# Kernel optimization log

Measured on AMD Instinct MI355X. Metric: run time of the kernel, lower is better.

Reference implementation:

```python
import jax, jax.numpy as jnp
import numpy as np

H, DK, DIM, DFF, DEPTH = 8, 64, 512, 2048, 8
B, LS, LT, VOCAB = 16, 128, 128, 32000


def setup_inputs() -> dict:
    key = jax.random.key(0)
    ks = jax.random.split(key, 20)
    w = lambda k, s: jax.random.normal(k, s, jnp.float32) * 0.02
    N_enc, N_dec = B * LS, B * LT
    base_s = np.arange(B) * LS
    base_t = np.arange(B) * LT
    i = np.arange(LS)
    j = np.arange(LT)
    # encoder self-attn: full bipartite within each sentence
    ee_src = (base_s[:, None, None] + i[None, :, None] + 0 * i[None, None, :]).reshape(-1)
    ee_dst = (base_s[:, None, None] + 0 * i[None, :, None] + i[None, None, :]).reshape(-1)
    # decoder self-attn: causal (key pos <= query pos)
    ii, jj = np.meshgrid(j, j, indexing='ij')  # ii = dst(query) pos, jj = src(key) pos
    m = jj <= ii
    dd_src = (base_t[:, None] + jj[m][None, :]).reshape(-1)
    dd_dst = (base_t[:, None] + ii[m][None, :]).reshape(-1)
    # cross-attn: enc node -> dec node, full within sentence
    ed_src = (base_s[:, None, None] + i[None, :, None] + 0 * j[None, None, :]).reshape(-1)
    ed_dst = (base_t[:, None, None] + 0 * i[None, :, None] + j[None, None, :]).reshape(-1)
    return {
        'emb_src': w(ks[0], (VOCAB, DIM)), 'emb_tgt': w(ks[1], (VOCAB, DIM)),
        'pos_emb': w(ks[2], (LS, DIM)), 'time_emb': w(ks[3], (DEPTH, DIM)),
        'Wqkv_e': w(ks[4], (DIM, 3 * DIM)), 'Wo_e': w(ks[5], (DIM, DIM)),
        'W1_e': w(ks[6], (DIM, DFF)), 'W2_e': w(ks[7], (DFF, DIM)),
        'Wqkv_d': w(ks[8], (DIM, 3 * DIM)), 'Wo_d': w(ks[9], (DIM, DIM)),
        'W1_d': w(ks[10], (DIM, DFF)), 'W2_d': w(ks[11], (DFF, DIM)),
        'Wq_x': w(ks[12], (DIM, DIM)), 'Wkv_x': w(ks[13], (DIM, 2 * DIM)),
        'Wo_x': w(ks[14], (DIM, DIM)), 'Wgen': w(ks[15], (DIM, VOCAB)),
        'src_tokens': jax.random.randint(ks[16], (N_enc,), 0, VOCAB, jnp.int32),
        'tgt_tokens': jax.random.randint(ks[17], (N_dec,), 0, VOCAB, jnp.int32),
        'src_pos': jnp.tile(jnp.arange(LS, dtype=jnp.int32), B),
        'tgt_pos': jnp.tile(jnp.arange(LT, dtype=jnp.int32), B),
        'ee_src': jnp.asarray(ee_src, jnp.int32), 'ee_dst': jnp.asarray(ee_dst, jnp.int32),
        'dd_src': jnp.asarray(dd_src, jnp.int32), 'dd_dst': jnp.asarray(dd_dst, jnp.int32),
        'ed_src': jnp.asarray(ed_src, jnp.int32), 'ed_dst': jnp.asarray(ed_dst, jnp.int32),
    }


def _ln(x):
    m = x.mean(-1, keepdims=True)
    v = ((x - m) ** 2).mean(-1, keepdims=True)
    return (x - m) * jax.lax.rsqrt(v + 1e-5)


def _attn(q, k, v, src, dst, n_dst):
    # q: [Nq,H,DK] (dst side), k/v: [Nk,H,DK] (src side); edge lists [E]
    # src_dot_dst -> scaled_exp -> scatter-sum (src_mul_edge + sum, copy_edge + sum), then wv/z
    s = jnp.exp(jnp.einsum('ehd,ehd->eh', k[src], q[dst]) / np.float32(np.sqrt(DK)))  # [E,H]
    wv = jax.ops.segment_sum(s[:, :, None] * v[src], dst, num_segments=n_dst)  # [Nq,H,DK]
    z = jax.ops.segment_sum(s, dst, num_segments=n_dst)  # [Nq,H]
    return (wv / (z[:, :, None] + 1e-9)).reshape(n_dst, DIM)


def reference(emb_src, emb_tgt, pos_emb, time_emb, Wqkv_e, Wo_e, W1_e, W2_e,
              Wqkv_d, Wo_d, W1_d, W2_d, Wq_x, Wkv_x, Wo_x, Wgen,
              src_tokens, tgt_tokens, src_pos, tgt_pos,
              ee_src, ee_dst, dd_src, dd_dst, ed_src, ed_dst):
    Ne, Nd = src_tokens.shape[0], tgt_tokens.shape[0]
    x_e = emb_src[src_tokens] + pos_emb[src_pos]
    x_d = emb_tgt[tgt_tokens] + pos_emb[tgt_pos]
    # encoder: MAX_DEPTH shared-weight iterations with time+pos enc re-added each step
    for t in range(DEPTH):
        xp = x_e + pos_emb[src_pos] + time_emb[t]
        q, k, v = jnp.split(xp @ Wqkv_e, 3, axis=-1)
        o = _attn(q.reshape(Ne, H, DK), k.reshape(Ne, H, DK), v.reshape(Ne, H, DK), ee_src, ee_dst, Ne)
        x_e = _ln(x_e + o @ Wo_e)
        x_e = _ln(x_e + jax.nn.relu(x_e @ W1_e) @ W2_e)
    # decoder: self-attn (causal dd) then cross-attn (ed) each iteration
    for t in range(DEPTH):
        xp = x_d + pos_emb[tgt_pos] + time_emb[t]
        q, k, v = jnp.split(xp @ Wqkv_d, 3, axis=-1)
        o = _attn(q.reshape(Nd, H, DK), k.reshape(Nd, H, DK), v.reshape(Nd, H, DK), dd_src, dd_dst, Nd)
        x_d = _ln(x_d + o @ Wo_d)
        qx = ((x_d + pos_emb[tgt_pos] + time_emb[t]) @ Wq_x).reshape(Nd, H, DK)
        kx, vx = jnp.split(x_e @ Wkv_x, 2, axis=-1)
        o = _attn(qx, kx.reshape(Ne, H, DK), vx.reshape(Ne, H, DK), ed_src, ed_dst, Nd)
        x_d = _ln(x_d + o @ Wo_x)
        x_d = _ln(x_d + jax.nn.relu(x_d @ W1_d) @ W2_d)
    return jax.nn.log_softmax(x_d @ Wgen, axis=-1)  # generator over dec nodes
```

## Files before the change

kernel.cpp:

```cpp
#include <hip/hip_runtime.h>
#include <hip/hip_bf16.h>
#include <math.h>

#define H 8
#define DK 64
#define DIM 512
#define DFF 2048
#define DEPTH 8
#define VOCAB 32000
#define NTOK 2048

typedef float f32x4 __attribute__((ext_vector_type(4)));
typedef short bf16x8 __attribute__((ext_vector_type(8)));

static __device__ __forceinline__ unsigned short f2bf(float f) {
    unsigned u = __float_as_uint(f);
    return (unsigned short)((u + 0x7FFFu + ((u >> 16) & 1u)) >> 16);
}

#define GLL(src, dst) __builtin_amdgcn_global_load_lds( \
    (const __attribute__((address_space(1))) unsigned int*)(src), \
    (__attribute__((address_space(3))) unsigned int*)(dst), 16, 0, 0)

__global__ void embed_kernel(const float* __restrict__ emb, const int* __restrict__ tok,
                             const float* __restrict__ pos, const int* __restrict__ pidx,
                             float* __restrict__ out, int n4) {
    int idx = blockIdx.x * blockDim.x + threadIdx.x;
    if (idx >= n4) return;
    int i = idx >> 7, d = idx & 127;
    float4 a = ((const float4*)emb)[(size_t)tok[i] * 128 + d];
    float4 b = ((const float4*)pos)[(size_t)pidx[i] * 128 + d];
    ((float4*)out)[idx] = make_float4(a.x + b.x, a.y + b.y, a.z + b.z, a.w + b.w);
}

struct WD { const float* src; unsigned short* dst; int K; int N; int t0; int pad; };
struct WTab { WD d[12]; };

__global__ __launch_bounds__(256) void wconv_all(WTab tab) {
    __shared__ float t[32][33];
    const int bid = blockIdx.x;
    int w = 0;
#pragma unroll
    for (int i = 1; i < 12; i++) if (bid >= tab.d[i].t0) w = i;
    const float* W = tab.d[w].src;
    unsigned short* Wt = tab.d[w].dst;
    const int K = tab.d[w].K, N = tab.d[w].N;
    const int lt = bid - tab.d[w].t0;
    const int txc = N >> 5;
    const int n0 = (lt % txc) << 5, k0 = (lt / txc) << 5;
    const int tid = threadIdx.x;
    const int tx = tid & 31, ty = tid >> 5;
#pragma unroll
    for (int i = 0; i < 32; i += 8)
        t[ty + i][tx] = W[(size_t)(k0 + ty + i) * N + n0 + tx];
    __syncthreads();
#pragma unroll
    for (int i = 0; i < 32; i += 8)
        Wt[(size_t)(n0 + ty + i) * K + k0 + tx] = f2bf(t[tx][ty + i]);
}

template<int EPI>
__global__ __launch_bounds__(256) void gemm_rb(
    const unsigned short* __restrict__ A,
    const unsigned short* __restrict__ Bt,
    unsigned short* __restrict__ Cb,
    int M, int N, int K)
{
    __shared__ __align__(16) unsigned short Asm[128 * 64];
    __shared__ __align__(16) unsigned short Bsm[128 * 64];
    const int tid = threadIdx.x;
    const int lane = tid & 63, wid = tid >> 6;
    const int m0 = blockIdx.y * 128, n0 = blockIdx.x * 128;
    const int wm = (wid >> 1) * 64, wn = (wid & 1) * 64;

    f32x4 acc[4][4];
#pragma unroll
    for (int i = 0; i < 4; i++)
#pragma unroll
        for (int j = 0; j < 4; j++) acc[i][j] = (f32x4){0.f, 0.f, 0.f, 0.f};

    for (int k0 = 0; k0 < K; k0 += 64) {
        if (k0) __syncthreads();
#pragma unroll
        for (int it = 0; it < 4; it++) {
            int q = (wid * 4 + it) * 64 + lane;
            int row = q >> 3;
            int cs = (q & 7) ^ (row & 7);
            GLL(Bt + (size_t)(n0 + row) * K + k0 + cs * 8, &Bsm[(wid * 4 + it) * 512]);
            GLL(A + (size_t)(m0 + row) * K + k0 + cs * 8, &Asm[(wid * 4 + it) * 512]);
        }
        __syncthreads();
#pragma unroll
        for (int kk = 0; kk < 2; kk++) {
            bf16x8 af[4], bfr[4];
#pragma unroll
            for (int i = 0; i < 4; i++) {
                int rowA = wm + i * 16 + (lane & 15);
                int ca = (kk * 4 + (lane >> 4)) ^ (rowA & 7);
                af[i] = *(const bf16x8*)&Asm[rowA * 64 + ca * 8];
                int rowB = wn + i * 16 + (lane & 15);
                int cb = (kk * 4 + (lane >> 4)) ^ (rowB & 7);
                bfr[i] = *(const bf16x8*)&Bsm[rowB * 64 + cb * 8];
            }
#pragma unroll
            for (int i = 0; i < 4; i++)
#pragma unroll
                for (int j = 0; j < 4; j++)
                    acc[i][j] = __builtin_amdgcn_mfma_f32_16x16x32_bf16(af[i], bfr[j], acc[i][j], 0, 0, 0);
        }
    }
#pragma unroll
    for (int i = 0; i < 4; i++)
#pragma unroll
        for (int j = 0; j < 4; j++)
#pragma unroll
            for (int r = 0; r < 4; r++) {
                int row = m0 + wm + i * 16 + (lane >> 4) * 4 + r;
                int col = n0 + wn + j * 16 + (lane & 15);
                size_t idx = (size_t)row * N + col;
                float v = acc[i][j][r];
                if (EPI == 1) Cb[idx] = f2bf(fmaxf(v, 0.f));
                if (EPI == 3) Cb[idx] = f2bf(v);
            }
}

__global__ __launch_bounds__(256) void gemm_bb(
    const unsigned short* __restrict__ A,
    const unsigned short* __restrict__ Bt,
    const float* __restrict__ R,
    float* __restrict__ Cf,
    int M, int N, int K)
{
    __shared__ __align__(16) unsigned short Asm[64 * 64];
    __shared__ __align__(16) unsigned short Bsm[64 * 64];
    const int tid = threadIdx.x;
    const int lane = tid & 63, wid = tid >> 6;
    const int m0 = blockIdx.y * 64, n0 = blockIdx.x * 64;
    const int wm = (wid >> 1) * 32, wn = (wid & 1) * 32;

    f32x4 acc[2][2];
#pragma unroll
    for (int i = 0; i < 2; i++)
#pragma unroll
        for (int j = 0; j < 2; j++) acc[i][j] = (f32x4){0.f, 0.f, 0.f, 0.f};

    for (int k0 = 0; k0 < K; k0 += 64) {
        if (k0) __syncthreads();
#pragma unroll
        for (int it = 0; it < 2; it++) {
            int q = it * 256 + tid;
            int row = q >> 3;
            int cs = (q & 7) ^ (row & 7);
            GLL(A + (size_t)(m0 + row) * K + k0 + cs * 8, &Asm[(it * 256 + wid * 64) * 8]);
            GLL(Bt + (size_t)(n0 + row) * K + k0 + cs * 8, &Bsm[(it * 256 + wid * 64) * 8]);
        }
        __syncthreads();
#pragma unroll
        for (int kd = 0; kd < 2; kd++) {
            bf16x8 af[2], bfr[2];
#pragma unroll
            for (int i = 0; i < 2; i++) {
                int rowA = wm + i * 16 + (lane & 15);
                int ca = (kd * 4 + (lane >> 4)) ^ (rowA & 7);
                af[i] = *(const bf16x8*)&Asm[rowA * 64 + ca * 8];
                int rowB = wn + i * 16 + (lane & 15);
                int cb = (kd * 4 + (lane >> 4)) ^ (rowB & 7);
                bfr[i] = *(const bf16x8*)&Bsm[rowB * 64 + cb * 8];
            }
#pragma unroll
            for (int i = 0; i < 2; i++)
#pragma unroll
                for (int j = 0; j < 2; j++)
                    acc[i][j] = __builtin_amdgcn_mfma_f32_16x16x32_bf16(af[i], bfr[j], acc[i][j], 0, 0, 0);
        }
    }
#pragma unroll
    for (int i = 0; i < 2; i++)
#pragma unroll
        for (int j = 0; j < 2; j++)
#pragma unroll
            for (int r = 0; r < 4; r++) {
                int row = m0 + wm + i * 16 + (lane >> 4) * 4 + r;
                int col = n0 + wn + j * 16 + (lane & 15);
                size_t idx = (size_t)row * N + col;
                Cf[idx] = acc[i][j][r] + R[idx];
            }
}

__global__ __launch_bounds__(64) void ln_kernel(const float* __restrict__ in,
                                                float* __restrict__ out,
                                                unsigned short* __restrict__ outb) {
    const int row = blockIdx.x, lane = threadIdx.x;
    const float* p = in + (size_t)row * DIM;
    float x[8];
#pragma unroll
    for (int i = 0; i < 8; i++) x[i] = p[lane + i * 64];
    float s = 0.f;
#pragma unroll
    for (int i = 0; i < 8; i++) s += x[i];
#pragma unroll
    for (int off = 32; off > 0; off >>= 1) s += __shfl_xor(s, off);
    const float m = s * (1.f / 512.f);
    float v = 0.f;
#pragma unroll
    for (int i = 0; i < 8; i++) { float d = x[i] - m; v += d * d; }
#pragma unroll
    for (int off = 32; off > 0; off >>= 1) v += __shfl_xor(v, off);
    v *= (1.f / 512.f);
    const float inv = 1.f / sqrtf(v + 1e-5f);
    float* q = out + (size_t)row * DIM;
    unsigned short* qb = outb + (size_t)row * DIM;
#pragma unroll
    for (int i = 0; i < 8; i++) {
        float y = (x[i] - m) * inv;
        q[lane + i * 64] = y;
        qb[lane + i * 64] = f2bf(y);
    }
}

template<int CAUSAL>
static __device__ __forceinline__ void attn_core16(
    const unsigned short* Qs, const unsigned short* Ks, const unsigned short* Vt,
    unsigned short* Psw, int wq, int lane, int tok0, int h,
    unsigned short* __restrict__ O)
{
    bf16x8 qa[2];
#pragma unroll
    for (int kd = 0; kd < 2; kd++) {
        int qr = wq + (lane & 15);
        int ch = (kd * 4 + (lane >> 4)) ^ (qr & 7);
        qa[kd] = *(const bf16x8*)&Qs[qr * 64 + ch * 8];
    }
    const int kcmax = CAUSAL ? ((wq >> 5) + 1) : 4;
    const int jmax = CAUSAL ? (kcmax * 2) : 8;

    float zr[4] = {0.f, 0.f, 0.f, 0.f};
    f32x4 oacc[4];
#pragma unroll
    for (int dt = 0; dt < 4; dt++) oacc[dt] = (f32x4){0.f, 0.f, 0.f, 0.f};

    for (int kb = 0; kb < 2; kb++) {
        int j0 = kb * 4;
        if (j0 >= jmax) break;
        int jn = jmax - j0; if (jn > 4) jn = 4;
        f32x4 sacc[4];
#pragma unroll
        for (int j = 0; j < 4; j++) sacc[j] = (f32x4){0.f, 0.f, 0.f, 0.f};
#pragma unroll 2
        for (int kd = 0; kd < 2; kd++) {
            for (int jj = 0; jj < jn; jj++) {
                int kr = (j0 + jj) * 16 + (lane & 15);
                int ch = (kd * 4 + (lane >> 4)) ^ (kr & 7);
                bf16x8 kf = *(const bf16x8*)&Ks[kr * 64 + ch * 8];
                sacc[jj] = __builtin_amdgcn_mfma_f32_16x16x32_bf16(qa[kd], kf, sacc[jj], 0, 0, 0);
            }
        }
        int qbase = wq + (lane >> 4) * 4;
        for (int jj = 0; jj < jn; jj++) {
            int kcol = (j0 + jj) * 16 + (lane & 15);
#pragma unroll
            for (int rr = 0; rr < 4; rr++) {
                float p = __expf(sacc[jj][rr] * 0.125f);
                if (CAUSAL && kcol > qbase + rr) p = 0.f;
                zr[rr] += p;
                int prow = (lane >> 4) * 4 + rr;
                int ch = ((jj * 2 + ((lane & 15) >> 3)) ^ (prow & 7));
                Psw[prow * 64 + ch * 8 + (lane & 7)] = f2bf(p);
            }
        }
        int kcn = kcmax - kb * 2; if (kcn > 2) kcn = 2;
        for (int kcl = 0; kcl < kcn; kcl++) {
            bf16x8 pa;
            {
                int prow = lane & 15;
                int ch = (kcl * 4 + (lane >> 4)) ^ (prow & 7);
                pa = *(const bf16x8*)&Psw[prow * 64 + ch * 8];
            }
            int kcg = kb * 2 + kcl;
#pragma unroll
            for (int dt = 0; dt < 4; dt++) {
                int d = dt * 16 + (lane & 15);
                bf16x8 vf = *(const bf16x8*)&Vt[d * 132 + (kcg * 4 + (lane >> 4)) * 8];
                oacc[dt] = __builtin_amdgcn_mfma_f32_16x16x32_bf16(pa, vf, oacc[dt], 0, 0, 0);
            }
        }
    }
#pragma unroll
    for (int rr = 0; rr < 4; rr++) {
        float z = zr[rr];
        z += __shfl_xor(z, 1); z += __shfl_xor(z, 2);
        z += __shfl_xor(z, 4); z += __shfl_xor(z, 8);
        zr[rr] = 1.f / (z + 1e-9f);
    }
#pragma unroll
    for (int dt = 0; dt < 4; dt++)
#pragma unroll
        for (int rr = 0; rr < 4; rr++) {
            int qrow = tok0 + wq + (lane >> 4) * 4 + rr;
            O[(size_t)qrow * DIM + h * 64 + dt * 16 + (lane & 15)] =
                f2bf(oacc[dt][rr] * zr[rr]);
        }
}

template<int CAUSAL>
__global__ __launch_bounds__(512) void fused_attn(
    const float* __restrict__ Xf,
    const float* __restrict__ pos,
    const float* __restrict__ trow,
    const unsigned short* __restrict__ WqkvT,
    unsigned short* __restrict__ O)
{
    __shared__ __align__(16) unsigned short smem[33024];
    unsigned short* Asm = smem;
    unsigned short* Bsm = smem + 8192;
    unsigned short* Qs  = smem;
    unsigned short* Ks  = smem + 8192;
    unsigned short* Vt  = smem + 16384;
    const int tid = threadIdx.x;
    const int lane = tid & 63, wid = tid >> 6;
    unsigned short* Psw = smem + 24832 + wid * 1024;
    const int b = blockIdx.x >> 3, h = blockIdx.x & 7;
    const int tok0 = b * 128;
    const int wq = wid * 16;

    f32x4 acc[12];
#pragma unroll
    for (int c = 0; c < 12; c++) acc[c] = (f32x4){0.f, 0.f, 0.f, 0.f};

    for (int k0 = 0; k0 < 512; k0 += 64) {
        if (k0) __syncthreads();
#pragma unroll
        for (int it = 0; it < 3; it++) {
            int q = it * 512 + wid * 64 + lane;
            int r = q >> 3;
            int cs = (q & 7) ^ (r & 7);
            int srow = (r < 64) ? (h * 64 + r)
                     : (r < 128) ? (512 + h * 64 + (r - 64))
                                 : (1024 + h * 64 + (r - 128));
            GLL(WqkvT + (size_t)srow * 512 + k0 + cs * 8, &Bsm[(it * 512 + wid * 64) * 8]);
        }
#pragma unroll
        for (int it = 0; it < 2; it++) {
            int q = it * 512 + tid;
            int row = q >> 3;
            int cs = q & 7;
            const float* s = Xf + (size_t)(tok0 + row) * 512 + k0 + cs * 8;
            const float* pp = pos + (size_t)row * 512 + k0 + cs * 8;
            const float* tt = trow + k0 + cs * 8;
            float4 u0 = *(const float4*)s, u1 = *(const float4*)(s + 4);
            float4 p0 = *(const float4*)pp, p1 = *(const float4*)(pp + 4);
            float4 t0 = *(const float4*)tt, t1 = *(const float4*)(tt + 4);
            u0.x += p0.x + t0.x; u0.y += p0.y + t0.y; u0.z += p0.z + t0.z; u0.w += p0.w + t0.w;
            u1.x += p1.x + t1.x; u1.y += p1.y + t1.y; u1.z += p1.z + t1.z; u1.w += p1.w + t1.w;
            unsigned short c8[8];
            c8[0] = f2bf(u0.x); c8[1] = f2bf(u0.y); c8[2] = f2bf(u0.z); c8[3] = f2bf(u0.w);
            c8[4] = f2bf(u1.x); c8[5] = f2bf(u1.y); c8[6] = f2bf(u1.z); c8[7] = f2bf(u1.w);
            *(bf16x8*)&Asm[row * 64 + ((cs ^ (row & 7)) * 8)] = *(bf16x8*)c8;
        }
        __syncthreads();
#pragma unroll
        for (int kk = 0; kk < 2; kk++) {
            int rowA = wq + (lane & 15);
            int ca = (kk * 4 + (lane >> 4)) ^ (rowA & 7);
            bf16x8 af = *(const bf16x8*)&Asm[rowA * 64 + ca * 8];
#pragma unroll
            for (int c = 0; c < 12; c++) {
                int rowB = c * 16 + (lane & 15);
                int cb = (kk * 4 + (lane >> 4)) ^ (rowB & 7);
                bf16x8 bfr = *(const bf16x8*)&Bsm[rowB * 64 + cb * 8];
                acc[c] = __builtin_amdgcn_mfma_f32_16x16x32_bf16(af, bfr, acc[c], 0, 0, 0);
            }
        }
    }
    __syncthreads();
#pragma unroll
    for (int c = 0; c < 12; c++)
#pragma unroll
        for (int r = 0; r < 4; r++) {
            int token = wq + (lane >> 4) * 4 + r;
            int col = (c & 3) * 16 + (lane & 15);
            unsigned short v = f2bf(acc[c][r]);
            if (c < 4)      Qs[token * 64 + (((col >> 3) ^ (token & 7)) * 8) + (col & 7)] = v;
            else if (c < 8) Ks[token * 64 + (((col >> 3) ^ (token & 7)) * 8) + (col & 7)] = v;
            else            Vt[col * 132 + token] = v;
        }
    __syncthreads();
    attn_core16<CAUSAL>(Qs, Ks, Vt, Psw, wq, lane, tok0, h, O);
}

__global__ __launch_bounds__(512) void fused_xattn(
    const float* __restrict__ Xf,
    const float* __restrict__ pos,
    const float* __restrict__ trow,
    const unsigned short* __restrict__ WqT,
    const unsigned short* __restrict__ kvx,
    unsigned short* __restrict__ O)
{
    __shared__ __align__(16) unsigned short smem[33024];
    unsigned short* Asm = smem;
    unsigned short* Bsm = smem + 8192;
    unsigned short* Qs  = smem;
    unsigned short* Ks  = smem + 8192;
    unsigned short* Vt  = smem + 16384;
    const int tid = threadIdx.x;
    const int lane = tid & 63, wid = tid >> 6;
    unsigned short* Psw = smem + 24832 + wid * 1024;
    const int b = blockIdx.x >> 3, h = blockIdx.x & 7;
    const int tok0 = b * 128;
    const int wq = wid * 16;

    f32x4 acc[4];
#pragma unroll
    for (int c = 0; c < 4; c++) acc[c] = (f32x4){0.f, 0.f, 0.f, 0.f};

    for (int k0 = 0; k0 < 512; k0 += 64) {
        if (k0) __syncthreads();
        {
            int q = wid * 64 + lane;
            int r = q >> 3;
            int cs = (q & 7) ^ (r & 7);
            GLL(WqT + (size_t)(h * 64 + r) * 512 + k0 + cs * 8, &Bsm[(wid * 64) * 8]);
        }
#pragma unroll
        for (int it = 0; it < 2; it++) {
            int q = it * 512 + tid;
            int row = q >> 3;
            int cs = q & 7;
            const float* s = Xf + (size_t)(tok0 + row) * 512 + k0 + cs * 8;
            const float* pp = pos + (size_t)row * 512 + k0 + cs * 8;
            const float* tt = trow + k0 + cs * 8;
            float4 u0 = *(const float4*)s, u1 = *(const float4*)(s + 4);
            float4 p0 = *(const float4*)pp, p1 = *(const float4*)(pp + 4);
            float4 t0 = *(const float4*)tt, t1 = *(const float4*)(tt + 4);
            u0.x += p0.x + t0.x; u0.y += p0.y + t0.y; u0.z += p0.z + t0.z; u0.w += p0.w + t0.w;
            u1.x += p1.x + t1.x; u1.y += p1.y + t1.y; u1.z += p1.z + t1.z; u1.w += p1.w + t1.w;
            unsigned short c8[8];
            c8[0] = f2bf(u0.x); c8[1] = f2bf(u0.y); c8[2] = f2bf(u0.z); c8[3] = f2bf(u0.w);
            c8[4] = f2bf(u1.x); c8[5] = f2bf(u1.y); c8[6] = f2bf(u1.z); c8[7] = f2bf(u1.w);
            *(bf16x8*)&Asm[row * 64 + ((cs ^ (row & 7)) * 8)] = *(bf16x8*)c8;
        }
        __syncthreads();
#pragma unroll
        for (int kk = 0; kk < 2; kk++) {
            int rowA = wq + (lane & 15);
            int ca = (kk * 4 + (lane >> 4)) ^ (rowA & 7);
            bf16x8 af = *(const bf16x8*)&Asm[rowA * 64 + ca * 8];
#pragma unroll
            for (int c = 0; c < 4; c++) {
                int rowB = c * 16 + (lane & 15);
                int cb = (kk * 4 + (lane >> 4)) ^ (rowB & 7);
                bf16x8 bfr = *(const bf16x8*)&Bsm[rowB * 64 + cb * 8];
                acc[c] = __builtin_amdgcn_mfma_f32_16x16x32_bf16(af, bfr, acc[c], 0, 0, 0);
            }
        }
    }
    __syncthreads();
#pragma unroll
    for (int c = 0; c < 4; c++)
#pragma unroll
        for (int r = 0; r < 4; r++) {
            int token = wq + (lane >> 4) * 4 + r;
            int col = c * 16 + (lane & 15);
            Qs[token * 64 + (((col >> 3) ^ (token & 7)) * 8) + (col & 7)] = f2bf(acc[c][r]);
        }
    {
        int r = tid >> 2, c0 = (tid & 3) * 2;
        const unsigned short* Kg = kvx + (size_t)(tok0 + r) * 1024 + h * 64;
        const unsigned short* Vg = Kg + 512;
#pragma unroll
        for (int c = c0; c < c0 + 2; c++) {
            bf16x8 kv = *(const bf16x8*)&Kg[c * 8];
            *(bf16x8*)&Ks[r * 64 + ((c ^ (r & 7)) * 8)] = kv;
            bf16x8 vv = *(const bf16x8*)&Vg[c * 8];
#pragma unroll
            for (int j = 0; j < 8; j++)
                Vt[(c * 8 + j) * 132 + r] = (unsigned short)vv[j];
        }
    }
    __syncthreads();
    attn_core16<0>(Qs, Ks, Vt, Psw, wq, lane, tok0, h, O);
}

__global__ __launch_bounds__(256) void gemm_gen(
    const unsigned short* __restrict__ Ab,
    const unsigned short* __restrict__ Bt,
    float* __restrict__ Out,
    float* __restrict__ pm,
    float* __restrict__ psum)
{
    __shared__ __align__(16) unsigned short Asm[128 * 64];
    __shared__ __align__(16) unsigned short Bsm[128 * 64];
    __shared__ float pml[4][64];
    __shared__ float psl[4][64];
    const int tid = threadIdx.x;
    const int lane = tid & 63, wid = tid >> 6;
    const int m0 = blockIdx.x * 128, n0 = blockIdx.y * 128;
    const int wm = (wid >> 1) * 64, wn = (wid & 1) * 64;

    f32x4 acc[4][4];
#pragma unroll
    for (int i = 0; i < 4; i++)
#pragma unroll
        for (int j = 0; j < 4; j++) acc[i][j] = (f32x4){0.f, 0.f, 0.f, 0.f};

    for (int k0 = 0; k0 < 512; k0 += 64) {
        if (k0) __syncthreads();
#pragma unroll
        for (int it = 0; it < 4; it++) {
            int q = (wid * 4 + it) * 64 + lane;
            int row = q >> 3;
            int cs = (q & 7) ^ (row & 7);
            GLL(Bt + (size_t)(n0 + row) * 512 + k0 + cs * 8, &Bsm[(wid * 4 + it) * 512]);
            GLL(Ab + (size_t)(m0 + row) * 512 + k0 + cs * 8, &Asm[(wid * 4 + it) * 512]);
        }
        __syncthreads();
#pragma unroll
        for (int kk = 0; kk < 2; kk++) {
            bf16x8 af[4], bfr[4];
#pragma unroll
            for (int i = 0; i < 4; i++) {
                int rowA = wm + i * 16 + (lane & 15);
                int ca = (kk * 4 + (lane >> 4)) ^ (rowA & 7);
                af[i] = *(const bf16x8*)&Asm[rowA * 64 + ca * 8];
                int rowB = wn + i * 16 + (lane & 15);
                int cb = (kk * 4 + (lane >> 4)) ^ (rowB & 7);
                bfr[i] = *(const bf16x8*)&Bsm[rowB * 64 + cb * 8];
            }
#pragma unroll
            for (int i = 0; i < 4; i++)
#pragma unroll
                for (int j = 0; j < 4; j++)
                    acc[i][j] = __builtin_amdgcn_mfma_f32_16x16x32_bf16(af[i], bfr[j], acc[i][j], 0, 0, 0);
        }
    }
#pragma unroll
    for (int i = 0; i < 4; i++) {
#pragma unroll
        for (int r = 0; r < 4; r++) {
            float mx = fmaxf(fmaxf(acc[i][0][r], acc[i][1][r]),
                             fmaxf(acc[i][2][r], acc[i][3][r]));
            mx = fmaxf(mx, __shfl_xor(mx, 1));
            mx = fmaxf(mx, __shfl_xor(mx, 2));
            mx = fmaxf(mx, __shfl_xor(mx, 4));
            mx = fmaxf(mx, __shfl_xor(mx, 8));
            float s = __expf(acc[i][0][r] - mx) + __expf(acc[i][1][r] - mx) +
                      __expf(acc[i][2][r] - mx) + __expf(acc[i][3][r] - mx);
            s += __shfl_xor(s, 1); s += __shfl_xor(s, 2);
            s += __shfl_xor(s, 4); s += __shfl_xor(s, 8);
            if ((lane & 15) == 0) {
                int li = i * 16 + (lane >> 4) * 4 + r;
                pml[wid][li] = mx;
                psl[wid][li] = s;
            }
        }
    }
    __syncthreads();
    if (tid < 128) {
        int half = tid >> 6, lr = tid & 63;
        int wa = half * 2, wb = half * 2 + 1;
        float ma = pml[wa][lr], mb = pml[wb][lr];
        float m = fmaxf(ma, mb);
        float s = psl[wa][lr] * __expf(ma - m) + psl[wb][lr] * __expf(mb - m);
        pm[(size_t)(m0 + tid) * 256 + blockIdx.y] = m;
        psum[(size_t)(m0 + tid) * 256 + blockIdx.y] = s;
    }
#pragma unroll
    for (int i = 0; i < 4; i++)
#pragma unroll
        for (int j = 0; j < 4; j++)
#pragma unroll
            for (int r = 0; r < 4; r++) {
                int row = m0 + wm + i * 16 + (lane >> 4) * 4 + r;
                int col = n0 + wn + j * 16 + (lane & 15);
                Out[(size_t)row * VOCAB + col] = acc[i][j][r];
            }
}

__global__ __launch_bounds__(64) void lse_kernel(const float* __restrict__ pm,
                                                 const float* __restrict__ psum,
                                                 float* __restrict__ lse) {
    const int row = blockIdx.x, t = threadIdx.x;
    float m = -1e30f, s = 0.f;
    for (int nb = t; nb < 250; nb += 64) {
        float mm = pm[(size_t)row * 256 + nb];
        float ss = psum[(size_t)row * 256 + nb];
        float M = fmaxf(m, mm);
        s = s * __expf(m - M) + ss * __expf(mm - M);
        m = M;
    }
#pragma unroll
    for (int off = 32; off > 0; off >>= 1) {
        float mo = __shfl_xor(m, off), so = __shfl_xor(s, off);
        float M = fmaxf(m, mo);
        s = s * __expf(m - M) + so * __expf(mo - M);
        m = M;
    }
    if (t == 0) lse[row] = m + __logf(s);
}

__global__ __launch_bounds__(256) void sub_kernel(float* __restrict__ out,
                                                  const float* __restrict__ lse) {
    const int row = blockIdx.x;
    const float l = lse[row];
    float4* p = (float4*)(out + (size_t)row * VOCAB);
    for (int i = threadIdx.x; i < VOCAB / 4; i += 256) {
        float4 v = p[i];
        p[i] = make_float4(v.x - l, v.y - l, v.z - l, v.w - l);
    }
}

extern "C" void kernel_launch(void* const* d_in, const int* in_sizes, int n_in,
                              void* d_out, int out_size, void* d_ws, size_t ws_size,
                              hipStream_t stream) {
    const float* emb_src  = (const float*)d_in[0];
    const float* emb_tgt  = (const float*)d_in[1];
    const float* pos_emb  = (const float*)d_in[2];
    const float* time_emb = (const float*)d_in[3];
    const float* Wqkv_e   = (const float*)d_in[4];
    const float* Wo_e     = (const float*)d_in[5];
    const float* W1_e     = (const float*)d_in[6];
    const float* W2_e     = (const float*)d_in[7];
    const float* Wqkv_d   = (const float*)d_in[8];
    const float* Wo_d     = (const float*)d_in[9];
    const float* W1_d     = (const float*)d_in[10];
    const float* W2_d     = (const float*)d_in[11];
    const float* Wq_x     = (const float*)d_in[12];
    const float* Wkv_x    = (const float*)d_in[13];
    const float* Wo_x     = (const float*)d_in[14];
    const float* Wgen     = (const float*)d_in[15];
    const int* src_tokens = (const int*)d_in[16];
    const int* tgt_tokens = (const int*)d_in[17];
    const int* src_pos    = (const int*)d_in[18];
    const int* tgt_pos    = (const int*)d_in[19];

    char* w = (char*)d_ws;
    float* x_e = (float*)(w);
    float* x_d = (float*)(w + (4u << 20));
    float* tmp = (float*)(w + (8u << 20));
    unsigned short* kvx_bf = (unsigned short*)(w + (12u << 20));
    unsigned short* o_bf   = (unsigned short*)(w + (16u << 20));
    unsigned short* hid_bf = (unsigned short*)(w + (18u << 20));
    float* pm   = (float*)(w + (26u << 20));
    float* psum = (float*)(w + (28u << 20));
    float* lse  = (float*)(w + (30u << 20));
    unsigned short* xe_bf = (unsigned short*)(w + (31u << 20));
    unsigned short* xd_bf = (unsigned short*)(w + (33u << 20));
    unsigned short* wts   = (unsigned short*)(w + (35u << 20));

    unsigned short* WqkvE_t = wts;
    unsigned short* WoE_t   = WqkvE_t + 786432;
    unsigned short* W1E_t   = WoE_t   + 262144;
    unsigned short* W2E_t   = W1E_t   + 1048576;
    unsigned short* WqkvD_t = W2E_t   + 1048576;
    unsigned short* WoD_t   = WqkvD_t + 786432;
    unsigned short* W1D_t   = WoD_t   + 262144;
    unsigned short* W2D_t   = W1D_t   + 1048576;
    unsigned short* WqX_t   = W2D_t   + 1048576;
    unsigned short* WkvX_t  = WqX_t   + 262144;
    unsigned short* WoX_t   = WkvX_t  + 524288;
    unsigned short* Wgen_t  = WoX_t   + 262144;

    float* out = (float*)d_out;

    WTab tab;
    auto set = [&](int i, const float* s, unsigned short* d, int K, int N, int t0) {
        tab.d[i].src = s; tab.d[i].dst = d; tab.d[i].K = K; tab.d[i].N = N;
        tab.d[i].t0 = t0; tab.d[i].pad = 0;
    };
    set(0,  Wqkv_e, WqkvE_t, 512, 1536, 0);
    set(1,  Wo_e,   WoE_t,   512, 512,  768);
    set(2,  W1_e,   W1E_t,   512, 2048, 1024);
    set(3,  W2_e,   W2E_t,   2048, 512, 2048);
    set(4,  Wqkv_d, WqkvD_t, 512, 1536, 3072);
    set(5,  Wo_d,   WoD_t,   512, 512,  3840);
    set(6,  W1_d,   W1D_t,   512, 2048, 4096);
    set(7,  W2_d,   W2D_t,   2048, 512, 5120);
    set(8,  Wq_x,   WqX_t,   512, 512,  6144);
    set(9,  Wkv_x,  WkvX_t,  512, 1024, 6400);
    set(10, Wo_x,   WoX_t,   512, 512,  6912);
    set(11, Wgen,   Wgen_t,  512, 32000, 7168);
    wconv_all<<<23168, 256, 0, stream>>>(tab);

    const int n4 = NTOK * (DIM / 4);
    dim3 eb(256), eg((n4 + 255) / 256);
    embed_kernel<<<eg, eb, 0, stream>>>(emb_src, src_tokens, pos_emb, src_pos, x_e, n4);
    embed_kernel<<<eg, eb, 0, stream>>>(emb_tgt, tgt_tokens, pos_emb, tgt_pos, x_d, n4);

    const dim3 gFF(DFF / 128, NTOK / 128), gKV(1024 / 128, NTOK / 128),
               g64(512 / 64, NTOK / 64);

    for (int t = 0; t < DEPTH; t++) {
        const float* trow = time_emb + (size_t)t * DIM;
        fused_attn<0><<<128, 512, 0, stream>>>(x_e, pos_emb, trow, WqkvE_t, o_bf);
        gemm_bb<<<g64, 256, 0, stream>>>(o_bf, WoE_t, x_e, tmp, NTOK, 512, 512);
        ln_kernel<<<NTOK, 64, 0, stream>>>(tmp, x_e, xe_bf);
        gemm_rb<1><<<gFF, 256, 0, stream>>>(xe_bf, W1E_t, hid_bf, NTOK, DFF, 512);
        gemm_bb<<<g64, 256, 0, stream>>>(hid_bf, W2E_t, x_e, tmp, NTOK, 512, 2048);
        ln_kernel<<<NTOK, 64, 0, stream>>>(tmp, x_e, xe_bf);
    }

    gemm_rb<3><<<gKV, 256, 0, stream>>>(xe_bf, WkvX_t, kvx_bf, NTOK, 1024, 512);

    for (int t = 0; t < DEPTH; t++) {
        const float* trow = time_emb + (size_t)t * DIM;
        fused_attn<1><<<128, 512, 0, stream>>>(x_d, pos_emb, trow, WqkvD_t, o_bf);
        gemm_bb<<<g64, 256, 0, stream>>>(o_bf, WoD_t, x_d, tmp, NTOK, 512, 512);
        ln_kernel<<<NTOK, 64, 0, stream>>>(tmp, x_d, xd_bf);

        fused_xattn<<<128, 512, 0, stream>>>(x_d, pos_emb, trow, WqX_t, kvx_bf, o_bf);
        gemm_bb<<<g64, 256, 0, stream>>>(o_bf, WoX_t, x_d, tmp, NTOK, 512, 512);
        ln_kernel<<<NTOK, 64, 0, stream>>>(tmp, x_d, xd_bf);

        gemm_rb<1><<<gFF, 256, 0, stream>>>(xd_bf, W1D_t, hid_bf, NTOK, DFF, 512);
        gemm_bb<<<g64, 256, 0, stream>>>(hid_bf, W2D_t, x_d, tmp, NTOK, 512, 2048);
        ln_kernel<<<NTOK, 64, 0, stream>>>(tmp, x_d, xd_bf);
    }

    gemm_gen<<<dim3(16, 250), 256, 0, stream>>>(xd_bf, Wgen_t, out, pm, psum);
    lse_kernel<<<NTOK, 64, 0, stream>>>(pm, psum, lse);
    sub_kernel<<<NTOK, 256, 0, stream>>>(out, lse);
}
```

Measured before the change: 1.855 ms.

## Fold LayerNorm into GEMM epilogues/prologues via per-block row statistics

Removes the standalone LayerNorm kernels by having each residual GEMM write the un-normalized sum plus per-row partial sum and sum-of-squares. Consumers apply normalization on the fly when loading A tiles. The generator GEMM moves to 256-row tiles with 512 threads, and the lse and subtract kernels are merged into one. This saves many launches and round trips over the activations, at the cost of a single-pass variance that is less numerically stable and extra fp32 A-tile conversion in the FFN GEMM.

New measurement: 1.857 ms. Within noise of the previous version (+0.1%).

```diff
diff --git a/kernel.cpp b/kernel.cpp
--- a/kernel.cpp
+++ b/kernel.cpp
@@ -21,6 +21,25 @@
 #define GLL(src, dst) __builtin_amdgcn_global_load_lds( \
     (const __attribute__((address_space(1))) unsigned int*)(src), \
     (__attribute__((address_space(3))) unsigned int*)(dst), 16, 0, 0)
+
+static __device__ __forceinline__ void load_ln_stats(
+    const float* __restrict__ stats, int base, int rows,
+    float* Lm, float* Li, int tid, int nthr)
+{
+    for (int r = tid; r < rows; r += nthr) {
+        float m = 0.f, inv = 1.f;
+        if (stats) {
+            const float* s = stats + (size_t)(base + r) * 16;
+            float sum = 0.f, sq = 0.f;
+#pragma unroll
+            for (int b = 0; b < 8; b++) { sum += s[b * 2]; sq += s[b * 2 + 1]; }
+            m = sum * (1.f / 512.f);
+            float v = sq * (1.f / 512.f) - m * m;
+            inv = 1.f / sqrtf(v + 1e-5f);
+        }
+        Lm[r] = m; Li[r] = inv;
+    }
+}
 
 __global__ void embed_kernel(const float* __restrict__ emb, const int* __restrict__ tok,
                              const float* __restrict__ pos, const int* __restrict__ pidx,
@@ -61,17 +80,22 @@
 
 template<int EPI>
 __global__ __launch_bounds__(256) void gemm_rb(
-    const unsigned short* __restrict__ A,
+    const float* __restrict__ Tf,
+    const float* __restrict__ stats,
     const unsigned short* __restrict__ Bt,
     unsigned short* __restrict__ Cb,
     int M, int N, int K)
 {
     __shared__ __align__(16) unsigned short Asm[128 * 64];
     __shared__ __align__(16) unsigned short Bsm[128 * 64];
+    __shared__ float Lm[128], Li[128];
     const int tid = threadIdx.x;
     const int lane = tid & 63, wid = tid >> 6;
     const int m0 = blockIdx.y * 128, n0 = blockIdx.x * 128;
     const int wm = (wid >> 1) * 64, wn = (wid & 1) * 64;
+
+    load_ln_stats(stats, m0, 128, Lm, Li, tid, 256);
+    __syncthreads();
 
     f32x4 acc[4][4];
 #pragma unroll
@@ -87,7 +111,21 @@
             int row = q >> 3;
             int cs = (q & 7) ^ (row & 7);
             GLL(Bt + (size_t)(n0 + row) * K + k0 + cs * 8, &Bsm[(wid * 4 + it) * 512]);
-            GLL(A + (size_t)(m0 + row) * K + k0 + cs * 8, &Asm[(wid * 4 + it) * 512]);
+        }
+#pragma unroll
+        for (int it = 0; it < 4; it++) {
+            int q = (wid * 4 + it) * 64 + lane;
+            int row = q >> 3;
+            int cs = q & 7;
+            const float* s = Tf + (size_t)(m0 + row) * K + k0 + cs * 8;
+            float4 u0 = *(const float4*)s, u1 = *(const float4*)(s + 4);
+            float m = Lm[row], iv = Li[row];
+            unsigned short c8[8];
+            c8[0] = f2bf((u0.x - m) * iv); c8[1] = f2bf((u0.y - m) * iv);
+            c8[2] = f2bf((u0.z - m) * iv); c8[3] = f2bf((u0.w - m) * iv);
+            c8[4] = f2bf((u1.x - m) * iv); c8[5] = f2bf((u1.y - m) * iv);
+            c8[6] = f2bf((u1.z - m) * iv); c8[7] = f2bf((u1.w - m) * iv);
+            *(bf16x8*)&Asm[row * 64 + ((cs ^ (row & 7)) * 8)] = *(bf16x8*)c8;
         }
         __syncthreads();
 #pragma unroll
@@ -127,16 +165,24 @@
 __global__ __launch_bounds__(256) void gemm_bb(
     const unsigned short* __restrict__ A,
     const unsigned short* __restrict__ Bt,
-    const float* __restrict__ R,
-    float* __restrict__ Cf,
-    int M, int N, int K)
+    const float* __restrict__ Tin,
+    const float* __restrict__ statsIn,
+    float* __restrict__ Tout,
+    float* __restrict__ statsOut,
+    int M, int K)
 {
     __shared__ __align__(16) unsigned short Asm[64 * 64];
     __shared__ __align__(16) unsigned short Bsm[64 * 64];
+    __shared__ float Lm[64], Li[64];
+    __shared__ float sredS[4][64], sredQ[4][64];
     const int tid = threadIdx.x;
     const int lane = tid & 63, wid = tid >> 6;
-    const int m0 = blockIdx.y * 64, n0 = blockIdx.x * 64;
+    const int nb = blockIdx.x;
+    const int m0 = blockIdx.y * 64, n0 = nb * 64;
     const int wm = (wid >> 1) * 32, wn = (wid & 1) * 32;
+
+    load_ln_stats(statsIn, m0, 64, Lm, Li, tid, 256);
+    __syncthreads();
 
     f32x4 acc[2][2];
 #pragma unroll
@@ -175,46 +221,36 @@
         }
     }
 #pragma unroll
-    for (int i = 0; i < 2; i++)
-#pragma unroll
-        for (int j = 0; j < 2; j++)
-#pragma unroll
-            for (int r = 0; r < 4; r++) {
-                int row = m0 + wm + i * 16 + (lane >> 4) * 4 + r;
+    for (int i = 0; i < 2; i++) {
+#pragma unroll
+        for (int r = 0; r < 4; r++) {
+            int rl = wm + i * 16 + (lane >> 4) * 4 + r;
+            int row = m0 + rl;
+            float s = 0.f, q = 0.f;
+#pragma unroll
+            for (int j = 0; j < 2; j++) {
                 int col = n0 + wn + j * 16 + (lane & 15);
-                size_t idx = (size_t)row * N + col;
-                Cf[idx] = acc[i][j][r] + R[idx];
-            }
-}
-
-__global__ __launch_bounds__(64) void ln_kernel(const float* __restrict__ in,
-                                                float* __restrict__ out,
-                                                unsigned short* __restrict__ outb) {
-    const int row = blockIdx.x, lane = threadIdx.x;
-    const float* p = in + (size_t)row * DIM;
-    float x[8];
-#pragma unroll
-    for (int i = 0; i < 8; i++) x[i] = p[lane + i * 64];
-    float s = 0.f;
-#pragma unroll
-    for (int i = 0; i < 8; i++) s += x[i];
-#pragma unroll
-    for (int off = 32; off > 0; off >>= 1) s += __shfl_xor(s, off);
-    const float m = s * (1.f / 512.f);
-    float v = 0.f;
-#pragma unroll
-    for (int i = 0; i < 8; i++) { float d = x[i] - m; v += d * d; }
-#pragma unroll
-    for (int off = 32; off > 0; off >>= 1) v += __shfl_xor(v, off);
-    v *= (1.f / 512.f);
-    const float inv = 1.f / sqrtf(v + 1e-5f);
-    float* q = out + (size_t)row * DIM;
-    unsigned short* qb = outb + (size_t)row * DIM;
-#pragma unroll
-    for (int i = 0; i < 8; i++) {
-        float y = (x[i] - m) * inv;
-        q[lane + i * 64] = y;
-        qb[lane + i * 64] = f2bf(y);
+                size_t idx = (size_t)row * DIM + col;
+                float rv = (Tin[idx] - Lm[rl]) * Li[rl];
+                float v = acc[i][j][r] + rv;
+                Tout[idx] = v;
+                s += v; q += v * v;
+            }
+            s += __shfl_xor(s, 1); s += __shfl_xor(s, 2);
+            s += __shfl_xor(s, 4); s += __shfl_xor(s, 8);
+            q += __shfl_xor(q, 1); q += __shfl_xor(q, 2);
+            q += __shfl_xor(q, 4); q += __shfl_xor(q, 8);
+            if ((lane & 15) == 0) { sredS[wid][rl] = s; sredQ[wid][rl] = q; }
+        }
+    }
+    __syncthreads();
+    if (tid < 64) {
+        int row = tid;
+        int w0 = (row >= 32) ? 2 : 0;
+        float s = sredS[w0][row] + sredS[w0 + 1][row];
+        float q = sredQ[w0][row] + sredQ[w0 + 1][row];
+        statsOut[(size_t)(m0 + row) * 16 + nb * 2] = s;
+        statsOut[(size_t)(m0 + row) * 16 + nb * 2 + 1] = q;
     }
 }
 
@@ -304,13 +340,15 @@
 
 template<int CAUSAL>
 __global__ __launch_bounds__(512) void fused_attn(
-    const float* __restrict__ Xf,
+    const float* __restrict__ Tf,
+    const float* __restrict__ stats,
     const float* __restrict__ pos,
     const float* __restrict__ trow,
     const unsigned short* __restrict__ WqkvT,
     unsigned short* __restrict__ O)
 {
     __shared__ __align__(16) unsigned short smem[33024];
+    __shared__ float LmA[128], LiA[128];
     unsigned short* Asm = smem;
     unsigned short* Bsm = smem + 8192;
     unsigned short* Qs  = smem;
@@ -323,6 +361,9 @@
     const int tok0 = b * 128;
     const int wq = wid * 16;
 
+    load_ln_stats(stats, tok0, 128, LmA, LiA, tid, 512);
+    __syncthreads();
+
     f32x4 acc[12];
 #pragma unroll
     for (int c = 0; c < 12; c++) acc[c] = (f32x4){0.f, 0.f, 0.f, 0.f};
@@ -344,17 +385,22 @@
             int q = it * 512 + tid;
             int row = q >> 3;
             int cs = q & 7;
-            const float* s = Xf + (size_t)(tok0 + row) * 512 + k0 + cs * 8;
+            const float* s = Tf + (size_t)(tok0 + row) * 512 + k0 + cs * 8;
             const float* pp = pos + (size_t)row * 512 + k0 + cs * 8;
             const float* tt = trow + k0 + cs * 8;
             float4 u0 = *(const float4*)s, u1 = *(const float4*)(s + 4);
             float4 p0 = *(const float4*)pp, p1 = *(const float4*)(pp + 4);
             float4 t0 = *(const float4*)tt, t1 = *(const float4*)(tt + 4);
-            u0.x += p0.x + t0.x; u0.y += p0.y + t0.y; u0.z += p0.z + t0.z; u0.w += p0.w + t0.w;
-            u1.x += p1.x + t1.x; u1.y += p1.y + t1.y; u1.z += p1.z + t1.z; u1.w += p1.w + t1.w;
+            float m = LmA[row], iv = LiA[row];
             unsigned short c8[8];
-            c8[0] = f2bf(u0.x); c8[1] = f2bf(u0.y); c8[2] = f2bf(u0.z); c8[3] = f2bf(u0.w);
-            c8[4] = f2bf(u1.x); c8[5] = f2bf(u1.y); c8[6] = f2bf(u1.z); c8[7] = f2bf(u1.w);
+            c8[0] = f2bf((u0.x - m) * iv + p0.x + t0.x);
+            c8[1] = f2bf((u0.y - m) * iv + p0.y + t0.y);
+            c8[2] = f2bf((u0.z - m) * iv + p0.z + t0.z);
+            c8[3] = f2bf((u0.w - m) * iv + p0.w + t0.w);
+            c8[4] = f2bf((u1.x - m) * iv + p1.x + t1.x);
+            c8[5] = f2bf((u1.y - m) * iv + p1.y + t1.y);
+            c8[6] = f2bf((u1.z - m) * iv + p1.z + t1.z);
+            c8[7] = f2bf((u1.w - m) * iv + p1.w + t1.w);
             *(bf16x8*)&Asm[row * 64 + ((cs ^ (row & 7)) * 8)] = *(bf16x8*)c8;
         }
         __syncthreads();
@@ -389,7 +435,8 @@
 }
 
 __global__ __launch_bounds__(512) void fused_xattn(
-    const float* __restrict__ Xf,
+    const float* __restrict__ Tf,
+    const float* __restrict__ stats,
     const float* __restrict__ pos,
     const float* __restrict__ trow,
     const unsigned short* __restrict__ WqT,
@@ -397,6 +444,7 @@
     unsigned short* __restrict__ O)
 {
     __shared__ __align__(16) unsigned short smem[33024];
+    __shared__ float LmA[128], LiA[128];
     unsigned short* Asm = smem;
     unsigned short* Bsm = smem + 8192;
     unsigned short* Qs  = smem;
@@ -409,6 +457,9 @@
     const int tok0 = b * 128;
     const int wq = wid * 16;
 
+    load_ln_stats(stats, tok0, 128, LmA, LiA, tid, 512);
+    __syncthreads();
+
     f32x4 acc[4];
 #pragma unroll
     for (int c = 0; c < 4; c++) acc[c] = (f32x4){0.f, 0.f, 0.f, 0.f};
@@ -426,17 +477,22 @@
             int q = it * 512 + tid;
             int row = q >> 3;
             int cs = q & 7;
-            const float* s = Xf + (size_t)(tok0 + row) * 512 + k0 + cs * 8;
+            const float* s = Tf + (size_t)(tok0 + row) * 512 + k0 + cs * 8;
             const float* pp = pos + (size_t)row * 512 + k0 + cs * 8;
             const float* tt = trow + k0 + cs * 8;
             float4 u0 = *(const float4*)s, u1 = *(const float4*)(s + 4);
             float4 p0 = *(const float4*)pp, p1 = *(const float4*)(pp + 4);
             float4 t0 = *(const float4*)tt, t1 = *(const float4*)(tt + 4);
-            u0.x += p0.x + t0.x; u0.y += p0.y + t0.y; u0.z += p0.z + t0.z; u0.w += p0.w + t0.w;
-            u1.x += p1.x + t1.x; u1.y += p1.y + t1.y; u1.z += p1.z + t1.z; u1.w += p1.w + t1.w;
+            float m = LmA[row], iv = LiA[row];
             unsigned short c8[8];
-            c8[0] = f2bf(u0.x); c8[1] = f2bf(u0.y); c8[2] = f2bf(u0.z); c8[3] = f2bf(u0.w);
-            c8[4] = f2bf(u1.x); c8[5] = f2bf(u1.y); c8[6] = f2bf(u1.z); c8[7] = f2bf(u1.w);
+            c8[0] = f2bf((u0.x - m) * iv + p0.x + t0.x);
+            c8[1] = f2bf((u0.y - m) * iv + p0.y + t0.y);
+            c8[2] = f2bf((u0.z - m) * iv + p0.z + t0.z);
+            c8[3] = f2bf((u0.w - m) * iv + p0.w + t0.w);
+            c8[4] = f2bf((u1.x - m) * iv + p1.x + t1.x);
+            c8[5] = f2bf((u1.y - m) * iv + p1.y + t1.y);
+            c8[6] = f2bf((u1.z - m) * iv + p1.z + t1.z);
+            c8[7] = f2bf((u1.w - m) * iv + p1.w + t1.w);
             *(bf16x8*)&Asm[row * 64 + ((cs ^ (row & 7)) * 8)] = *(bf16x8*)c8;
         }
         __syncthreads();
@@ -481,20 +537,38 @@
     attn_core16<0>(Qs, Ks, Vt, Psw, wq, lane, tok0, h, O);
 }
 
-__global__ __launch_bounds__(256) void gemm_gen(
+__global__ __launch_bounds__(64) void ln_fin(const float* __restrict__ T,
+                                             const float* __restrict__ stats,
+                                             unsigned short* __restrict__ outb) {
+    const int row = blockIdx.x, lane = threadIdx.x;
+    const float* st = stats + (size_t)row * 16;
+    float sum = 0.f, sq = 0.f;
+#pragma unroll
+    for (int b = 0; b < 8; b++) { sum += st[b * 2]; sq += st[b * 2 + 1]; }
+    float m = sum * (1.f / 512.f);
+    float v = sq * (1.f / 512.f) - m * m;
+    float inv = 1.f / sqrtf(v + 1e-5f);
+    const float* p = T + (size_t)row * DIM;
+    unsigned short* qb = outb + (size_t)row * DIM;
+#pragma unroll
+    for (int i = 0; i < 8; i++)
+        qb[lane + i * 64] = f2bf((p[lane + i * 64] - m) * inv);
+}
+
+__global__ __launch_bounds__(512) void gemm_gen(
     const unsigned short* __restrict__ Ab,
     const unsigned short* __restrict__ Bt,
     float* __restrict__ Out,
     float* __restrict__ pm,
     float* __restrict__ psum)
 {
-    __shared__ __align__(16) unsigned short Asm[128 * 64];
+    __shared__ __align__(16) unsigned short Asm[256 * 64];
     __shared__ __align__(16) unsigned short Bsm[128 * 64];
-    __shared__ float pml[4][64];
-    __shared__ float psl[4][64];
+    __shared__ float pml[8][64];
+    __shared__ float psl[8][64];
     const int tid = threadIdx.x;
     const int lane = tid & 63, wid = tid >> 6;
-    const int m0 = blockIdx.x * 128, n0 = blockIdx.y * 128;
+    const int m0 = blockIdx.x * 256, n0 = blockIdx.y * 128;
     const int wm = (wid >> 1) * 64, wn = (wid & 1) * 64;
 
     f32x4 acc[4][4];
@@ -506,12 +580,18 @@
     for (int k0 = 0; k0 < 512; k0 += 64) {
         if (k0) __syncthreads();
 #pragma unroll
-        for (int it = 0; it < 4; it++) {
-            int q = (wid * 4 + it) * 64 + lane;
+        for (int it = 0; it < 2; it++) {
+            int q = it * 512 + tid;
             int row = q >> 3;
             int cs = (q & 7) ^ (row & 7);
-            GLL(Bt + (size_t)(n0 + row) * 512 + k0 + cs * 8, &Bsm[(wid * 4 + it) * 512]);
-            GLL(Ab + (size_t)(m0 + row) * 512 + k0 + cs * 8, &Asm[(wid * 4 + it) * 512]);
+            GLL(Bt + (size_t)(n0 + row) * 512 + k0 + cs * 8, &Bsm[(it * 512 + wid * 64) * 8]);
+        }
+#pragma unroll
+        for (int it = 0; it < 4; it++) {
+            int q = it * 512 + tid;
+            int row = q >> 3;
+            int cs = (q & 7) ^ (row & 7);
+            GLL(Ab + (size_t)(m0 + row) * 512 + k0 + cs * 8, &Asm[(it * 512 + wid * 64) * 8]);
         }
         __syncthreads();
 #pragma unroll
@@ -555,14 +635,14 @@
         }
     }
     __syncthreads();
-    if (tid < 128) {
-        int half = tid >> 6, lr = tid & 63;
-        int wa = half * 2, wb = half * 2 + 1;
+    if (tid < 256) {
+        int g = tid >> 6, lr = tid & 63;
+        int wa = g * 2, wb = g * 2 + 1;
         float ma = pml[wa][lr], mb = pml[wb][lr];
         float m = fmaxf(ma, mb);
         float s = psl[wa][lr] * __expf(ma - m) + psl[wb][lr] * __expf(mb - m);
-        pm[(size_t)(m0 + tid) * 256 + blockIdx.y] = m;
-        psum[(size_t)(m0 + tid) * 256 + blockIdx.y] = s;
+        pm[(size_t)(m0 + g * 64 + lr) * 256 + blockIdx.y] = m;
+        psum[(size_t)(m0 + g * 64 + lr) * 256 + blockIdx.y] = s;
     }
 #pragma unroll
     for (int i = 0; i < 4; i++)
@@ -576,16 +656,18 @@
             }
 }
 
-__global__ __launch_bounds__(64) void lse_kernel(const float* __restrict__ pm,
-                                                 const float* __restrict__ psum,
-                                                 float* __restrict__ lse) {
-    const int row = blockIdx.x, t = threadIdx.x;
+__global__ __launch_bounds__(256) void sub_kernel(float* __restrict__ out,
+                                                  const float* __restrict__ pm,
+                                                  const float* __restrict__ psum) {
+    const int row = blockIdx.x, tid = threadIdx.x;
+    const int lane = tid & 63, wid = tid >> 6;
+    __shared__ float ms[4], ss[4];
     float m = -1e30f, s = 0.f;
-    for (int nb = t; nb < 250; nb += 64) {
+    for (int nb = tid; nb < 250; nb += 256) {
         float mm = pm[(size_t)row * 256 + nb];
-        float ss = psum[(size_t)row * 256 + nb];
+        float sv = psum[(size_t)row * 256 + nb];
         float M = fmaxf(m, mm);
-        s = s * __expf(m - M) + ss * __expf(mm - M);
+        s = s * __expf(m - M) + sv * __expf(mm - M);
         m = M;
     }
 #pragma unroll
@@ -595,17 +677,16 @@
         s = s * __expf(m - M) + so * __expf(mo - M);
         m = M;
     }
-    if (t == 0) lse[row] = m + __logf(s);
-}
-
-__global__ __launch_bounds__(256) void sub_kernel(float* __restrict__ out,
-                                                  const float* __restrict__ lse) {
-    const int row = blockIdx.x;
-    const float l = lse[row];
+    if (lane == 0) { ms[wid] = m; ss[wid] = s; }
+    __syncthreads();
+    float M = fmaxf(fmaxf(ms[0], ms[1]), fmaxf(ms[2], ms[3]));
+    float S = ss[0] * __expf(ms[0] - M) + ss[1] * __expf(ms[1] - M) +
+              ss[2] * __expf(ms[2] - M) + ss[3] * __expf(ms[3] - M);
+    const float lse = M + __logf(S);
     float4* p = (float4*)(out + (size_t)row * VOCAB);
-    for (int i = threadIdx.x; i < VOCAB / 4; i += 256) {
+    for (int i = tid; i < VOCAB / 4; i += 256) {
         float4 v = p[i];
-        p[i] = make_float4(v.x - l, v.y - l, v.z - l, v.w - l);
+        p[i] = make_float4(v.x - lse, v.y - lse, v.z - lse, v.w - lse);
     }
 }
 
@@ -634,18 +715,23 @@
     const int* tgt_pos    = (const int*)d_in[19];
 
     char* w = (char*)d_ws;
-    float* x_e = (float*)(w);
-    float* x_d = (float*)(w + (4u << 20));
-    float* tmp = (float*)(w + (8u << 20));
-    unsigned short* kvx_bf = (unsigned short*)(w + (12u << 20));
-    unsigned short* o_bf   = (unsigned short*)(w + (16u << 20));
-    unsigned short* hid_bf = (unsigned short*)(w + (18u << 20));
-    float* pm   = (float*)(w + (26u << 20));
-    float* psum = (float*)(w + (28u << 20));
-    float* lse  = (float*)(w + (30u << 20));
-    unsigned short* xe_bf = (unsigned short*)(w + (31u << 20));
-    unsigned short* xd_bf = (unsigned short*)(w + (33u << 20));
-    unsigned short* wts   = (unsigned short*)(w + (35u << 20));
+    float* T_e0 = (float*)(w);
+    float* T_e1 = (float*)(w + (4u << 20));
+    float* T_d0 = (float*)(w + (8u << 20));
+    float* T_d1 = (float*)(w + (12u << 20));
+    float* T_d2 = (float*)(w + (16u << 20));
+    unsigned short* kvx_bf = (unsigned short*)(w + (20u << 20));
+    unsigned short* o_bf   = (unsigned short*)(w + (24u << 20));
+    unsigned short* hid_bf = (unsigned short*)(w + (26u << 20));
+    unsigned short* xd_bf  = (unsigned short*)(w + (34u << 20));
+    float* pm   = (float*)(w + (36u << 20));
+    float* psum = (float*)(w + (38u << 20));
+    float* se0  = (float*)(w + (40u << 20));
+    float* se1  = se0 + 32768;
+    float* sd0  = se1 + 32768;
+    float* sd1  = sd0 + 32768;
+    float* sd2  = sd1 + 32768;
+    unsigned short* wts = (unsigned short*)(w + (41u << 20));
 
     unsigned short* WqkvE_t = wts;
     unsigned short* WoE_t   = WqkvE_t + 786432;
@@ -683,40 +769,43 @@
 
     const int n4 = NTOK * (DIM / 4);
     dim3 eb(256), eg((n4 + 255) / 256);
-    embed_kernel<<<eg, eb, 0, stream>>>(emb_src, src_tokens, pos_emb, src_pos, x_e, n4);
-    embed_kernel<<<eg, eb, 0, stream>>>(emb_tgt, tgt_tokens, pos_emb, tgt_pos, x_d, n4);
+    embed_kernel<<<eg, eb, 0, stream>>>(emb_src, src_tokens, pos_emb, src_pos, T_e0, n4);
+    embed_kernel<<<eg, eb, 0, stream>>>(emb_tgt, tgt_tokens, pos_emb, tgt_pos, T_d0, n4);
 
     const dim3 gFF(DFF / 128, NTOK / 128), gKV(1024 / 128, NTOK / 128),
-               g64(512 / 64, NTOK / 64);
-
-    for (int t = 0; t < DEPTH; t++) {
-        const float* trow = time_emb + (size_t)t * DIM;
-        fused_attn<0><<<128, 512, 0, stream>>>(x_e, pos_emb, trow, WqkvE_t, o_bf);
-        gemm_bb<<<g64, 256, 0, stream>>>(o_bf, WoE_t, x_e, tmp, NTOK, 512, 512);
-        ln_kernel<<<NTOK, 64, 0, stream>>>(tmp, x_e, xe_bf);
-        gemm_rb<1><<<gFF, 256, 0, stream>>>(xe_bf, W1E_t, hid_bf, NTOK, DFF, 512);
-        gemm_bb<<<g64, 256, 0, stream>>>(hid_bf, W2E_t, x_e, tmp, NTOK, 512, 2048);
-        ln_kernel<<<NTOK, 64, 0, stream>>>(tmp, x_e, xe_bf);
-    }
-
-    gemm_rb<3><<<gKV, 256, 0, stream>>>(xe_bf, WkvX_t, kvx_bf, NTOK, 1024, 512);
-
-    for (int t = 0; t < DEPTH; t++) {
-        const float* trow = time_emb + (size_t)t * DIM;
-        fused_attn<1><<<128, 512, 0, stream>>>(x_d, pos_emb, trow, WqkvD_t, o_bf);
-        gemm_bb<<<g64, 256, 0, stream>>>(o_bf, WoD_t, x_d, tmp, NTOK, 512, 512);
-        ln_kernel<<<NTOK, 64, 0, stream>>>(tmp, x_d, xd_bf);
-
-        fused_xattn<<<128, 512, 0, stream>>>(x_d, pos_emb, trow, WqX_t, kvx_bf, o_bf);
-        gemm_bb<<<g64, 256, 0, stream>>>(o_bf, WoX_t, x_d, tmp, NTOK, 512, 512);
-        ln_kernel<<<NTOK, 64, 0, stream>>>(tmp, x_d, xd_bf);
-
-        gemm_rb<1><<<gFF, 256, 0, stream>>>(xd_bf, W1D_t, hid_bf, NTOK, DFF, 512);
-        gemm_bb<<<g64, 256, 0, stream>>>(hid_bf, W2D_t, x_d, tmp, NTOK, 512, 2048);
-        ln_kernel<<<NTOK, 64, 0, stream>>>(tmp, x_d, xd_bf);
-    }
-
-    gemm_gen<<<dim3(16, 250), 256, 0, stream>>>(xd_bf, Wgen_t, out, pm, psum);
-    lse_kernel<<<NTOK, 64, 0, stream>>>(pm, psum, lse);
-    sub_kernel<<<NTOK, 256, 0, stream>>>(out, lse);
-}
+               gBB(8, NTOK / 64);
+
+    {
+        const float* scur = nullptr;
+        for (int t = 0; t < DEPTH; t++) {
+            const float* trow = time_emb + (size_t)t * DIM;
+            fused_attn<0><<<128, 512, 0, stream>>>(T_e0, scur, pos_emb, trow, WqkvE_t, o_bf);
+            gemm_bb<<<gBB, 256, 0, stream>>>(o_bf, WoE_t, T_e0, scur, T_e1, se0, NTOK, 512);
+            gemm_rb<1><<<gFF, 256, 0, stream>>>(T_e1, se0, W1E_t, hid_bf, NTOK, DFF, 512);
+            gemm_bb<<<gBB, 256, 0, stream>>>(hid_bf, W2E_t, T_e1, se0, T_e0, se1, NTOK, 2048);
+            scur = se1;
+        }
+    }
+
+    gemm_rb<3><<<gKV, 256, 0, stream>>>(T_e0, se1, WkvX_t, kvx_bf, NTOK, 1024, 512);
+
+    {
+        const float* scur = nullptr;
+        for (int t = 0; t < DEPTH; t++) {
+            const float* trow = time_emb + (size_t)t * DIM;
+            fused_attn<1><<<128, 512, 0, stream>>>(T_d0, scur, pos_emb, trow, WqkvD_t, o_bf);
+            gemm_bb<<<gBB, 256, 0, stream>>>(o_bf, WoD_t, T_d0, scur, T_d1, sd0, NTOK, 512);
+
+            fused_xattn<<<128, 512, 0, stream>>>(T_d1, sd0, pos_emb, trow, WqX_t, kvx_bf, o_bf);
+            gemm_bb<<<gBB, 256, 0, stream>>>(o_bf, WoX_t, T_d1, sd0, T_d2, sd1, NTOK, 512);
+
+            gemm_rb<1><<<gFF, 256, 0, stream>>>(T_d2, sd1, W1D_t, hid_bf, NTOK, DFF, 512);
+            gemm_bb<<<gBB, 256, 0, stream>>>(hid_bf, W2D_t, T_d2, sd1, T_d0, sd2, NTOK, 2048);
+            scur = sd2;
+        }
+    }
+
+    ln_fin<<<NTOK, 64, 0, stream>>>(T_d0, sd2, xd_bf);
+    gemm_gen<<<dim3(8, 250), 512, 0, stream>>>(xd_bf, Wgen_t, out, pm, psum);
+    sub_kernel<<<NTOK, 256, 0, stream>>>(out, pm, psum);
+}
```
